# Kernel tuning notes

Measured on AMD Instinct MI355X. Metric: run time of the kernel, lower is better.

Reference implementation:

```python
import jax, jax.numpy as jnp
import numpy as np

NUM_EXPERTS = 8
TOP_K = 2
D = 1024


def setup_inputs() -> dict:
    key = jax.random.key(0)
    ks = jax.random.split(key, 5)
    T = 16384
    x = jax.random.normal(ks[0], (T, D), dtype=jnp.float32)
    # torch nn.Linear params: weight [out, in], bias [out]
    Wg = jax.random.normal(ks[1], (NUM_EXPERTS, D), dtype=jnp.float32) * (1.0 / np.sqrt(D))
    bg = jnp.zeros((NUM_EXPERTS,), dtype=jnp.float32)
    We = jax.random.normal(ks[2], (NUM_EXPERTS, D, D), dtype=jnp.float32) * (1.0 / np.sqrt(D))
    be = jax.random.normal(ks[3], (NUM_EXPERTS, D), dtype=jnp.float32) * 0.01
    return {"x": x, "Wg": Wg, "bg": bg, "We": We, "be": be}


def reference(x, Wg, bg, We, be):
    T = x.shape[0]
    # gate logits [T, E]
    gate_logits = x @ Wg.T + bg
    top_k_gates, top_k_idx = jax.lax.top_k(gate_logits, TOP_K)  # [T, K]
    top_k_gates = jax.nn.softmax(top_k_gates, axis=-1)
    # dense per-expert combine weight: sum of gate probs where idx == e
    combine = jnp.zeros((T, NUM_EXPERTS), dtype=x.dtype)
    combine = combine.at[jnp.arange(T)[:, None], top_k_idx].add(top_k_gates)  # [T, E]
    # all-expert dense matmul (faithful to the original naive loop): [E, T, out]
    expert_out = jnp.einsum('td,eod->eto', x, We) + be[:, None, :]
    # weighted combine: output[t] = sum_e combine[t,e] * expert_out[e,t]
    out = jnp.einsum('te,eto->to', combine, expert_out)
    return out
```

## Files before the change

kernel.cpp:

```cpp
#include <hip/hip_runtime.h>
#include <hip/hip_bf16.h>
#include <stdint.h>

#define DDIM 1024
#define NEXP 8
#define SEG  16384

typedef __attribute__((ext_vector_type(8))) short bf16x8;
typedef __attribute__((ext_vector_type(4))) float f32x4;
typedef __attribute__((ext_vector_type(8))) unsigned short u16x8;

#define AS1 __attribute__((address_space(1)))
#define AS3 __attribute__((address_space(3)))

__device__ __forceinline__ unsigned short f2bf(float f) {
    union { float f; unsigned int u; } v; v.f = f;
    unsigned int u = v.u;
    return (unsigned short)((u + 0x7FFFu + ((u >> 16) & 1u)) >> 16);
}
__device__ __forceinline__ float bf2f(unsigned short h) {
    union { unsigned int u; float f; } v; v.u = ((unsigned int)h) << 16;
    return v.f;
}

__global__ __launch_bounds__(512) void prep(
    const float* __restrict__ x, const float* __restrict__ Wg,
    const float* __restrict__ bg, const float* __restrict__ We,
    unsigned short* __restrict__ xb, unsigned short* __restrict__ web,
    int* __restrict__ cnt, int* __restrict__ tok_list,
    float* __restrict__ gate_list) {

    __shared__ int   se[64];
    __shared__ float sg[64];

    if (blockIdx.x >= 512) {
        size_t idx = ((size_t)(blockIdx.x - 512) * 512 + threadIdx.x) * 8;
        const f32x4* p = (const f32x4*)(We + idx);
        f32x4 a = __builtin_nontemporal_load(p);
        f32x4 b = __builtin_nontemporal_load(p + 1);
        u16x8 h;
        h[0] = f2bf(a[0]); h[1] = f2bf(a[1]); h[2] = f2bf(a[2]); h[3] = f2bf(a[3]);
        h[4] = f2bf(b[0]); h[5] = f2bf(b[1]); h[6] = f2bf(b[2]); h[7] = f2bf(b[3]);
        *(u16x8*)(web + idx) = h;
        return;
    }

    int wave = threadIdx.x >> 6, lane = threadIdx.x & 63;
    int tbase = blockIdx.x * 32;

#pragma unroll
    for (int i = 0; i < 4; i++) {
        int lt = wave * 4 + i;
        int t = tbase + lt;
        const float* xr = x + (size_t)t * DDIM;
        int c0 = lane * 8;

        float4 v0 = ((const float4*)(xr + c0))[0];
        float4 v1 = ((const float4*)(xr + c0))[1];
        float4 v2 = ((const float4*)(xr + c0 + 512))[0];
        float4 v3 = ((const float4*)(xr + c0 + 512))[1];

        u16x8 h0, h1;
        h0[0] = f2bf(v0.x); h0[1] = f2bf(v0.y); h0[2] = f2bf(v0.z); h0[3] = f2bf(v0.w);
        h0[4] = f2bf(v1.x); h0[5] = f2bf(v1.y); h0[6] = f2bf(v1.z); h0[7] = f2bf(v1.w);
        h1[0] = f2bf(v2.x); h1[1] = f2bf(v2.y); h1[2] = f2bf(v2.z); h1[3] = f2bf(v2.w);
        h1[4] = f2bf(v3.x); h1[5] = f2bf(v3.y); h1[6] = f2bf(v3.z); h1[7] = f2bf(v3.w);
        *(u16x8*)(xb + (size_t)t * DDIM + c0) = h0;
        *(u16x8*)(xb + (size_t)t * DDIM + c0 + 512) = h1;

        float acc[NEXP];
#pragma unroll
        for (int e = 0; e < NEXP; e++) {
            const float* wr = Wg + e * DDIM;
            float4 w0 = ((const float4*)(wr + c0))[0];
            float4 w1 = ((const float4*)(wr + c0))[1];
            float4 w2 = ((const float4*)(wr + c0 + 512))[0];
            float4 w3 = ((const float4*)(wr + c0 + 512))[1];
            float s = v0.x*w0.x + v0.y*w0.y + v0.z*w0.z + v0.w*w0.w;
            s += v1.x*w1.x + v1.y*w1.y + v1.z*w1.z + v1.w*w1.w;
            s += v2.x*w2.x + v2.y*w2.y + v2.z*w2.z + v2.w*w2.w;
            s += v3.x*w3.x + v3.y*w3.y + v3.z*w3.z + v3.w*w3.w;
            acc[e] = s;
        }
#pragma unroll
        for (int e = 0; e < NEXP; e++) {
#pragma unroll
            for (int o = 32; o > 0; o >>= 1) acc[e] += __shfl_xor(acc[e], o, 64);
        }

        if (lane == 0) {
            float l1 = -1e30f, l2 = -1e30f; int e1 = 0, e2 = 0;
#pragma unroll
            for (int e = 0; e < NEXP; e++) {
                float le = acc[e] + bg[e];
                if (le > l1) { l2 = l1; e2 = e1; l1 = le; e1 = e; }
                else if (le > l2) { l2 = le; e2 = e; }
            }
            float g1 = 1.0f / (1.0f + __expf(l2 - l1));
            float g2 = 1.0f - g1;
            se[lt * 2]     = e1; sg[lt * 2]     = g1;
            se[lt * 2 + 1] = e2; sg[lt * 2 + 1] = g2;
        }
    }
    __syncthreads();

    if (threadIdx.x < NEXP) {
        int e = threadIdx.x;
        int k = 0;
#pragma unroll 8
        for (int i = 0; i < 64; i++) k += (se[i] == e);
        if (k) {
            int p = atomicAdd(cnt + e, k);
            for (int i = 0; i < 64; i++) {
                if (se[i] == e) {
                    tok_list[e * SEG + p]  = (tbase + (i >> 1)) * 2 + (i & 1);
                    gate_list[e * SEG + p] = sg[i];
                    p++;
                }
            }
        }
    }
}


__device__ __forceinline__ void stage_tile(const unsigned short* const* sp,
                                           unsigned short* lbase, int wave, int kt) {
    int ko = kt << 5;
#pragma unroll
    for (int j = 0; j < 3; ++j) {
        __builtin_amdgcn_global_load_lds(
            (const AS1 void*)(sp[j] + ko),
            (AS3 void*)(lbase + (wave * 3 + j) * 512),
            16, 0, 0);
    }
}

__device__ __forceinline__ void tile_mma(const unsigned short* ba, int aoff, int boff,
                                         f32x4 (&acc)[4][4]) {
    bf16x8 af[4], bf[4];
#pragma unroll
    for (int mi = 0; mi < 4; ++mi) af[mi] = *(const bf16x8*)(ba + aoff + mi * 512);
#pragma unroll
    for (int ni = 0; ni < 4; ++ni) bf[ni] = *(const bf16x8*)(ba + boff + ni * 512);
    __builtin_amdgcn_s_setprio(1);
#pragma unroll
    for (int mi = 0; mi < 4; ++mi)
#pragma unroll
        for (int ni = 0; ni < 4; ++ni)
            acc[mi][ni] = __builtin_amdgcn_mfma_f32_16x16x32_bf16(
                af[mi], bf[ni], acc[mi][ni], 0, 0, 0);
    __builtin_amdgcn_s_setprio(0);
}

template<bool STORE>
__global__ __launch_bounds__(512, 2) void moe_gemm(
    const unsigned short* __restrict__ xb, const unsigned short* __restrict__ web,
    const float* __restrict__ be, const int* __restrict__ cnt,
    const int* __restrict__ tok_list, const float* __restrict__ gate_list,
    unsigned short* __restrict__ Sb, float* __restrict__ outa) {

    extern __shared__ __align__(16) unsigned short lbuf[];
    __shared__ int   tok_s[128];
    __shared__ float gate_s[128];

    int id = blockIdx.y, e = 0, c = 0;
    while (e < NEXP) {
        c = cnt[e];
        int mt = (c + 127) >> 7;
        if (id < mt) break;
        id -= mt; e++;
    }
    if (e == NEXP) return;
    int m0 = id << 7;
    int n0 = blockIdx.x << 8;

    int tid = threadIdx.x;
    int w = tid >> 6, lane = tid & 63;
    int wave_m = w >> 2, wave_n = w & 3;

    if (tid < 128) {
        int r = m0 + tid;
        int rc = min(r, c - 1);
        tok_s[tid]  = tok_list[e * SEG + rc];
        gate_s[tid] = (r < c) ? gate_list[e * SEG + rc] : 0.0f;
    }
    __syncthreads();

    int mrow = lane & 15, q = lane >> 4;
    int ksl  = ((q + (mrow >> 1)) & 3) << 3;
    int aoff = (wave_m * 64 + mrow) * 32 + ksl;
    int boff = 4096 + (wave_n * 64 + mrow) * 32 + ksl;

    int g0  = ((lane & 3) - ((lane >> 3) & 3)) & 3;
    int sub = lane >> 2;
    const unsigned short* sp[3];
#pragma unroll
    for (int j = 0; j < 3; ++j) {
        int ch = w * 3 + j;
        int arow = min((ch << 4) + sub, 127);
        int brow = ((ch - 8) << 4) + sub;
        const unsigned short* pa = xb + (size_t)(tok_s[arow] >> 1) * DDIM + g0 * 8;
        const unsigned short* pb = web + ((size_t)e << 20) +
                                   (size_t)(n0 + brow) * DDIM + g0 * 8;
        sp[j] = (ch < 8) ? pa : pb;
    }

    f32x4 acc[4][4];
#pragma unroll
    for (int mi = 0; mi < 4; ++mi)
#pragma unroll
        for (int ni = 0; ni < 4; ++ni) acc[mi][ni] = (f32x4){0.f, 0.f, 0.f, 0.f};

    stage_tile(sp, lbuf,         w, 0);
    stage_tile(sp, lbuf + 12288, w, 1);

    for (int kb = 0; kb < 10; ++kb) {
#pragma unroll
        for (int u = 0; u < 3; ++u) {
            int kt = kb * 3 + u;
            asm volatile("s_waitcnt vmcnt(3)" ::: "memory");
            __builtin_amdgcn_s_barrier();
            asm volatile("" ::: "memory");
            stage_tile(sp, lbuf + ((u + 2) % 3) * 12288, w, kt + 2);
            tile_mma(lbuf + u * 12288, aoff, boff, acc);
        }
    }
    asm volatile("s_waitcnt vmcnt(3)" ::: "memory");
    __builtin_amdgcn_s_barrier();
    asm volatile("" ::: "memory");
    tile_mma(lbuf, aoff, boff, acc);

    asm volatile("s_waitcnt vmcnt(0)" ::: "memory");
    __builtin_amdgcn_s_barrier();
    asm volatile("" ::: "memory");
    tile_mma(lbuf + 12288, aoff, boff, acc);

    if (STORE) {
        __syncthreads();
#pragma unroll
        for (int ni = 0; ni < 4; ++ni) {
            int col = wave_n * 64 + ni * 16 + mrow;
            float bias = be[e * DDIM + n0 + col];
            int cg = col >> 3, cl = col & 7;
#pragma unroll
            for (int mi = 0; mi < 4; ++mi) {
#pragma unroll
                for (int r = 0; r < 4; ++r) {
                    int row = wave_m * 64 + mi * 16 + q * 4 + r;
                    lbuf[row * 256 + ((cg ^ (row & 7)) << 3) + cl] =
                        f2bf(gate_s[row] * (acc[mi][ni][r] + bias));
                }
            }
        }
        __syncthreads();
#pragma unroll
        for (int j = 0; j < 8; ++j) {
            int t = j * 512 + tid;
            int row = t >> 5, gc = t & 31;
            u16x8 vv = *(const u16x8*)&lbuf[row * 256 + ((gc ^ (row & 7)) << 3)];
            if (m0 + row < c)
                *(u16x8*)(Sb + (size_t)tok_s[row] * DDIM + n0 + gc * 8) = vv;
        }
    } else {
        __syncthreads();
#pragma unroll
        for (int ni = 0; ni < 4; ++ni) {
            int col = n0 + wave_n * 64 + ni * 16 + mrow;
            float bias = be[e * DDIM + col];
#pragma unroll
            for (int mi = 0; mi < 4; ++mi) {
#pragma unroll
                for (int r = 0; r < 4; ++r) {
                    int rl = wave_m * 64 + mi * 16 + q * 4 + r;
                    if (m0 + rl < c)
                        atomicAdd(outa + (size_t)(tok_s[rl] >> 1) * DDIM + col,
                                  gate_s[rl] * (acc[mi][ni][r] + bias));
                }
            }
        }
    }
}

__global__ void combine(const unsigned short* __restrict__ S, float* __restrict__ out) {
    size_t i = (size_t)blockIdx.x * 256 + threadIdx.x;
    size_t t = i >> 7;
    size_t g = i & 127;
    const u16x8* r0 = (const u16x8*)(S + t * 2 * DDIM) + g;
    const u16x8* r1 = (const u16x8*)(S + (t * 2 + 1) * DDIM) + g;
    u16x8 a = *r0;
    u16x8 b = *r1;
    f32x4 o0, o1;
#pragma unroll
    for (int k = 0; k < 4; k++) o0[k] = bf2f(a[k]) + bf2f(b[k]);
#pragma unroll
    for (int k = 0; k < 4; k++) o1[k] = bf2f(a[4 + k]) + bf2f(b[4 + k]);
    f32x4* op = (f32x4*)(out + t * DDIM + g * 8);
    __builtin_nontemporal_store(o0, op);
    __builtin_nontemporal_store(o1, op + 1);
}

extern "C" void kernel_launch(void* const* d_in, const int* in_sizes, int n_in,
                              void* d_out, int out_size, void* d_ws, size_t ws_size,
                              hipStream_t stream) {
    const float* x  = (const float*)d_in[0];
    const float* Wg = (const float*)d_in[1];
    const float* bg = (const float*)d_in[2];
    const float* We = (const float*)d_in[3];
    const float* be = (const float*)d_in[4];
    float* out = (float*)d_out;

    char* ws = (char*)d_ws;
    unsigned short* xb  = (unsigned short*)ws;
    unsigned short* web = (unsigned short*)(ws + 33554432);
    int*   tok_list  = (int*)(ws + 33554432 + 16777216);
    float* gate_list = (float*)(ws + 33554432 + 16777216 + 524288);
    int*   cnt       = (int*)(ws + 33554432 + 16777216 + 1048576);
    unsigned short* S = (unsigned short*)(ws + 52428800);

    const size_t NEED = 52428800ull + (size_t)32768 * DDIM * 2;

    static bool attr_done = false;
    if (!attr_done) {
        hipFuncSetAttribute(reinterpret_cast<const void*>(moe_gemm<true>),
                            hipFuncAttributeMaxDynamicSharedMemorySize, 73728);
        hipFuncSetAttribute(reinterpret_cast<const void*>(moe_gemm<false>),
                            hipFuncAttributeMaxDynamicSharedMemorySize, 73728);
        attr_done = true;
    }

    hipMemsetAsync(cnt, 0, NEXP * sizeof(int), stream);

    prep<<<2560, 512, 0, stream>>>(x, Wg, bg, We, xb, web, cnt, tok_list, gate_list);

    if (ws_size >= NEED) {
        moe_gemm<true><<<dim3(4, 264), 512, 73728, stream>>>(
            xb, web, be, cnt, tok_list, gate_list, S, nullptr);
        combine<<<8192, 256, 0, stream>>>(S, out);
    } else {
        hipMemsetAsync(d_out, 0, (size_t)out_size * sizeof(float), stream);
        moe_gemm<false><<<dim3(4, 264), 512, 73728, stream>>>(
            xb, web, be, cnt, tok_list, gate_list, nullptr, out);
    }
}
```

Before: 272.5 us.

## Enlarge MoE GEMM tile to 256x256 with XCD-aware block remapping

```diff
diff --git a/kernel.cpp b/kernel.cpp
--- a/kernel.cpp
+++ b/kernel.cpp
@@ -127,24 +127,24 @@
                                            unsigned short* lbase, int wave, int kt) {
     int ko = kt << 5;
 #pragma unroll
-    for (int j = 0; j < 3; ++j) {
+    for (int j = 0; j < 4; ++j) {
         __builtin_amdgcn_global_load_lds(
             (const AS1 void*)(sp[j] + ko),
-            (AS3 void*)(lbase + (wave * 3 + j) * 512),
+            (AS3 void*)(lbase + (wave * 4 + j) * 512),
             16, 0, 0);
     }
 }
 
 __device__ __forceinline__ void tile_mma(const unsigned short* ba, int aoff, int boff,
-                                         f32x4 (&acc)[4][4]) {
-    bf16x8 af[4], bf[4];
-#pragma unroll
-    for (int mi = 0; mi < 4; ++mi) af[mi] = *(const bf16x8*)(ba + aoff + mi * 512);
+                                         f32x4 (&acc)[8][4]) {
+    bf16x8 af[8], bf[4];
+#pragma unroll
+    for (int mi = 0; mi < 8; ++mi) af[mi] = *(const bf16x8*)(ba + aoff + mi * 512);
 #pragma unroll
     for (int ni = 0; ni < 4; ++ni) bf[ni] = *(const bf16x8*)(ba + boff + ni * 512);
     __builtin_amdgcn_s_setprio(1);
 #pragma unroll
-    for (int mi = 0; mi < 4; ++mi)
+    for (int mi = 0; mi < 8; ++mi)
 #pragma unroll
         for (int ni = 0; ni < 4; ++ni)
             acc[mi][ni] = __builtin_amdgcn_mfma_f32_16x16x32_bf16(
@@ -153,32 +153,35 @@
 }
 
 template<bool STORE>
-__global__ __launch_bounds__(512, 2) void moe_gemm(
+__global__ __launch_bounds__(512, 1) void moe_gemm(
     const unsigned short* __restrict__ xb, const unsigned short* __restrict__ web,
     const float* __restrict__ be, const int* __restrict__ cnt,
     const int* __restrict__ tok_list, const float* __restrict__ gate_list,
     unsigned short* __restrict__ Sb, float* __restrict__ outa) {
 
     extern __shared__ __align__(16) unsigned short lbuf[];
-    __shared__ int   tok_s[128];
-    __shared__ float gate_s[128];
-
-    int id = blockIdx.y, e = 0, c = 0;
+    __shared__ int   tok_s[256];
+    __shared__ float gate_s[256];
+
+    int fid = blockIdx.x + blockIdx.y * 4;
+    int L = (fid & 7) * 68 + (fid >> 3);
+
+    int e = 0, c = 0, rem = L;
     while (e < NEXP) {
         c = cnt[e];
-        int mt = (c + 127) >> 7;
-        if (id < mt) break;
-        id -= mt; e++;
+        int t_e = ((c + 255) >> 8) << 2;
+        if (rem < t_e) break;
+        rem -= t_e; e++;
     }
     if (e == NEXP) return;
-    int m0 = id << 7;
-    int n0 = blockIdx.x << 8;
+    int m0 = (rem >> 2) << 8;
+    int n0 = (rem & 3) << 8;
 
     int tid = threadIdx.x;
     int w = tid >> 6, lane = tid & 63;
     int wave_m = w >> 2, wave_n = w & 3;
 
-    if (tid < 128) {
+    if (tid < 256) {
         int r = m0 + tid;
         int rc = min(r, c - 1);
         tok_s[tid]  = tok_list[e * SEG + rc];
@@ -188,44 +191,44 @@
 
     int mrow = lane & 15, q = lane >> 4;
     int ksl  = ((q + (mrow >> 1)) & 3) << 3;
-    int aoff = (wave_m * 64 + mrow) * 32 + ksl;
-    int boff = 4096 + (wave_n * 64 + mrow) * 32 + ksl;
+    int aoff = (wave_m * 128 + mrow) * 32 + ksl;
+    int boff = 8192 + (wave_n * 64 + mrow) * 32 + ksl;
 
     int g0  = ((lane & 3) - ((lane >> 3) & 3)) & 3;
     int sub = lane >> 2;
-    const unsigned short* sp[3];
-#pragma unroll
-    for (int j = 0; j < 3; ++j) {
-        int ch = w * 3 + j;
-        int arow = min((ch << 4) + sub, 127);
-        int brow = ((ch - 8) << 4) + sub;
-        const unsigned short* pa = xb + (size_t)(tok_s[arow] >> 1) * DDIM + g0 * 8;
+    const unsigned short* sp[4];
+#pragma unroll
+    for (int j = 0; j < 4; ++j) {
+        int ch = w * 4 + j;
+        int arow = (ch << 4) + sub;
+        int brow = ((ch - 16) << 4) + sub;
+        const unsigned short* pa = xb + (size_t)(tok_s[arow & 255] >> 1) * DDIM + g0 * 8;
         const unsigned short* pb = web + ((size_t)e << 20) +
                                    (size_t)(n0 + brow) * DDIM + g0 * 8;
-        sp[j] = (ch < 8) ? pa : pb;
-    }
-
-    f32x4 acc[4][4];
-#pragma unroll
-    for (int mi = 0; mi < 4; ++mi)
+        sp[j] = (ch < 16) ? pa : pb;
+    }
+
+    f32x4 acc[8][4];
+#pragma unroll
+    for (int mi = 0; mi < 8; ++mi)
 #pragma unroll
         for (int ni = 0; ni < 4; ++ni) acc[mi][ni] = (f32x4){0.f, 0.f, 0.f, 0.f};
 
     stage_tile(sp, lbuf,         w, 0);
-    stage_tile(sp, lbuf + 12288, w, 1);
+    stage_tile(sp, lbuf + 16384, w, 1);
 
     for (int kb = 0; kb < 10; ++kb) {
 #pragma unroll
         for (int u = 0; u < 3; ++u) {
             int kt = kb * 3 + u;
-            asm volatile("s_waitcnt vmcnt(3)" ::: "memory");
+            asm volatile("s_waitcnt vmcnt(4)" ::: "memory");
             __builtin_amdgcn_s_barrier();
             asm volatile("" ::: "memory");
-            stage_tile(sp, lbuf + ((u + 2) % 3) * 12288, w, kt + 2);
-            tile_mma(lbuf + u * 12288, aoff, boff, acc);
-        }
-    }
-    asm volatile("s_waitcnt vmcnt(3)" ::: "memory");
+            stage_tile(sp, lbuf + ((u + 2) % 3) * 16384, w, kt + 2);
+            tile_mma(lbuf + u * 16384, aoff, boff, acc);
+        }
+    }
+    asm volatile("s_waitcnt vmcnt(4)" ::: "memory");
     __builtin_amdgcn_s_barrier();
     asm volatile("" ::: "memory");
     tile_mma(lbuf, aoff, boff, acc);
@@ -233,33 +236,39 @@
     asm volatile("s_waitcnt vmcnt(0)" ::: "memory");
     __builtin_amdgcn_s_barrier();
     asm volatile("" ::: "memory");
-    tile_mma(lbuf + 12288, aoff, boff, acc);
+    tile_mma(lbuf + 16384, aoff, boff, acc);
 
     if (STORE) {
         __syncthreads();
 #pragma unroll
-        for (int ni = 0; ni < 4; ++ni) {
-            int col = wave_n * 64 + ni * 16 + mrow;
-            float bias = be[e * DDIM + n0 + col];
-            int cg = col >> 3, cl = col & 7;
-#pragma unroll
-            for (int mi = 0; mi < 4; ++mi) {
-#pragma unroll
-                for (int r = 0; r < 4; ++r) {
-                    int row = wave_m * 64 + mi * 16 + q * 4 + r;
-                    lbuf[row * 256 + ((cg ^ (row & 7)) << 3) + cl] =
-                        f2bf(gate_s[row] * (acc[mi][ni][r] + bias));
+        for (int p = 0; p < 2; ++p) {
+            if (wave_m == p) {
+#pragma unroll
+                for (int ni = 0; ni < 4; ++ni) {
+                    int col = wave_n * 64 + ni * 16 + mrow;
+                    float bias = be[e * DDIM + n0 + col];
+                    int cg = col >> 3, cl = col & 7;
+#pragma unroll
+                    for (int mi = 0; mi < 8; ++mi) {
+#pragma unroll
+                        for (int r = 0; r < 4; ++r) {
+                            int row = mi * 16 + q * 4 + r;
+                            lbuf[row * 256 + ((cg ^ (row & 7)) << 3) + cl] =
+                                f2bf(gate_s[p * 128 + row] * (acc[mi][ni][r] + bias));
+                        }
+                    }
                 }
             }
-        }
-        __syncthreads();
-#pragma unroll
-        for (int j = 0; j < 8; ++j) {
-            int t = j * 512 + tid;
-            int row = t >> 5, gc = t & 31;
-            u16x8 vv = *(const u16x8*)&lbuf[row * 256 + ((gc ^ (row & 7)) << 3)];
-            if (m0 + row < c)
-                *(u16x8*)(Sb + (size_t)tok_s[row] * DDIM + n0 + gc * 8) = vv;
+            __syncthreads();
+#pragma unroll
+            for (int j = 0; j < 8; ++j) {
+                int t = j * 512 + tid;
+                int row = t >> 5, gc = t & 31;
+                u16x8 vv = *(const u16x8*)&lbuf[row * 256 + ((gc ^ (row & 7)) << 3)];
+                if (m0 + p * 128 + row < c)
+                    *(u16x8*)(Sb + (size_t)tok_s[p * 128 + row] * DDIM + n0 + gc * 8) = vv;
+            }
+            __syncthreads();
         }
     } else {
         __syncthreads();
@@ -268,10 +277,10 @@
             int col = n0 + wave_n * 64 + ni * 16 + mrow;
             float bias = be[e * DDIM + col];
 #pragma unroll
-            for (int mi = 0; mi < 4; ++mi) {
+            for (int mi = 0; mi < 8; ++mi) {
 #pragma unroll
                 for (int r = 0; r < 4; ++r) {
-                    int rl = wave_m * 64 + mi * 16 + q * 4 + r;
+                    int rl = wave_m * 128 + mi * 16 + q * 4 + r;
                     if (m0 + rl < c)
                         atomicAdd(outa + (size_t)(tok_s[rl] >> 1) * DDIM + col,
                                   gate_s[rl] * (acc[mi][ni][r] + bias));
@@ -322,9 +331,9 @@
     static bool attr_done = false;
     if (!attr_done) {
         hipFuncSetAttribute(reinterpret_cast<const void*>(moe_gemm<true>),
-                            hipFuncAttributeMaxDynamicSharedMemorySize, 73728);
+                            hipFuncAttributeMaxDynamicSharedMemorySize, 98304);
         hipFuncSetAttribute(reinterpret_cast<const void*>(moe_gemm<false>),
-                            hipFuncAttributeMaxDynamicSharedMemorySize, 73728);
+                            hipFuncAttributeMaxDynamicSharedMemorySize, 98304);
         attr_done = true;
     }
 
@@ -333,12 +342,12 @@
     prep<<<2560, 512, 0, stream>>>(x, Wg, bg, We, xb, web, cnt, tok_list, gate_list);
 
     if (ws_size >= NEED) {
-        moe_gemm<true><<<dim3(4, 264), 512, 73728, stream>>>(
+        moe_gemm<true><<<dim3(4, 136), 512, 98304, stream>>>(
             xb, web, be, cnt, tok_list, gate_list, S, nullptr);
         combine<<<8192, 256, 0, stream>>>(S, out);
     } else {
         hipMemsetAsync(d_out, 0, (size_t)out_size * sizeof(float), stream);
-        moe_gemm<false><<<dim3(4, 264), 512, 73728, stream>>>(
+        moe_gemm<false><<<dim3(4, 136), 512, 98304, stream>>>(
             xb, web, be, cnt, tok_list, gate_list, nullptr, out);
     }
 }
```

Result: slower. 290.4 us (+6.6%).
